# Performance work log

Hardware: AMD Instinct MI355X
Metric: run time of the kernel (lower is better)

Reference implementation:

```python
import jax, jax.numpy as jnp
import numpy as np

WS = 12      # window_size
OV = 6       # overlap
STEP = WS - OV
EPS = 1e-5   # LayerNorm eps (torch default)


def setup_inputs() -> dict:
    key = jax.random.key(0)
    ks = jax.random.split(key, 6)
    B, L, H, Dh = 4, 4092, 8, 64
    d_model = H * Dh
    sc = 1.0 / np.sqrt(Dh)
    return {
        "queries": jax.random.normal(ks[0], (B, L, H, Dh), dtype=jnp.float32),
        "keys": jax.random.normal(ks[1], (B, L, H, Dh), dtype=jnp.float32),
        "values": jax.random.normal(ks[2], (B, L, H, Dh), dtype=jnp.float32),
        "Wq": jax.random.normal(ks[3], (Dh, Dh), dtype=jnp.float32) * sc,
        "Wk": jax.random.normal(ks[4], (Dh, Dh), dtype=jnp.float32) * sc,
        "Wv": jax.random.normal(ks[5], (Dh, Dh), dtype=jnp.float32) * sc,
        "gamma": jnp.ones((d_model,), dtype=jnp.float32),
        "beta": jnp.zeros((d_model,), dtype=jnp.float32),
    }


def reference(queries, keys, values, Wq, Wk, Wv, gamma, beta):
    # input layout: [B, L, H, Dh]
    B, L, H, Dh = queries.shape
    nw = (L - OV) // STEP                       # number of windows
    Lc = WS + STEP * (nw - 1)                   # reconstructed length (== L)
    idx = jnp.arange(nw)[:, None] * STEP + jnp.arange(WS)[None, :]  # [nw, WS]

    def windows(x):
        # [B,L,H,Dh] -> [B,H,nw,WS,Dh]
        return jnp.transpose(x, (0, 2, 1, 3))[:, :, idx, :]

    qw, kw, vw = windows(queries), windows(keys), windows(values)
    # per-head-dim linear projections (nn.Linear: x @ W.T)
    Q = jnp.einsum('bhnwd,ed->bhnwe', qw, Wq)
    K = jnp.einsum('bhnwd,ed->bhnwe', kw, Wk)
    V = jnp.einsum('bhnwd,ed->bhnwe', vw, Wv)

    scores = jnp.einsum('bhnqd,bhnkd->bhnqk', Q, K) / jnp.sqrt(jnp.asarray(Dh, Q.dtype))
    attn = jax.nn.softmax(scores, axis=-1)      # [B,H,nw,WS,WS]
    ow = jnp.einsum('bhnqk,bhnkd->bhnqd', attn, V)

    # [B,H,nw,WS,Dh] -> [B,nw,WS,H*Dh]
    attn_out = jnp.transpose(ow, (0, 2, 3, 1, 4)).reshape(B, nw, WS, H * Dh)

    # overlap-add + averaging
    flat_idx = idx.reshape(-1)                  # [nw*WS]
    acc = jnp.zeros((B, Lc, H * Dh), dtype=attn_out.dtype)
    acc = acc.at[:, flat_idx, :].add(attn_out.reshape(B, nw * WS, H * Dh))
    cnt = jnp.zeros((Lc,), dtype=attn_out.dtype).at[flat_idx].add(1.0)
    out = acc / cnt[None, :, None]

    # residual + LayerNorm
    resid = queries.reshape(B, L, H * Dh)
    x = out + resid
    mu = jnp.mean(x, axis=-1, keepdims=True)
    var = jnp.mean((x - mu) ** 2, axis=-1, keepdims=True)
    z = (x - mu) / jnp.sqrt(var + EPS) * gamma + beta
    return z, attn
```

## Files before the change

kernel.cpp:

```cpp
#include <hip/hip_runtime.h>
#include <math.h>

#define B_    4
#define L_    4092
#define H_    8
#define DM    512
#define WS_   12
#define NW    681
#define NC    682
#define EPS_  1e-5f
#define Z_ELEMS (B_*L_*DM)
#define NQUAD 32736

typedef unsigned short u16;

__device__ __forceinline__ u16 f2bf(float f) {
    union { float f; unsigned u; } x; x.f = f;
    unsigned u = x.u;
    return (u16)((u + 0x7FFFu + ((u >> 16) & 1u)) >> 16);
}
__device__ __forceinline__ float bf2f(u16 h) {
    union { unsigned u; float f; } x; x.u = ((unsigned)h) << 16; return x.f;
}

__global__ __launch_bounds__(256) void proj_kernel(
    const float* __restrict__ q, const float* __restrict__ k, const float* __restrict__ v,
    const float* __restrict__ Wq, const float* __restrict__ Wk, const float* __restrict__ Wv,
    float* __restrict__ Qf, float* __restrict__ Kf, u16* __restrict__ Vh)
{
    const int tensor = blockIdx.y;
    const float* __restrict__ X = (tensor == 0) ? q  : (tensor == 1) ? k  : v;
    const float* __restrict__ W = (tensor == 0) ? Wq : (tensor == 1) ? Wk : Wv;
    float* __restrict__ Yf      = (tensor == 0) ? Qf : Kf;
    const bool isV = (tensor == 2);

    const int t = threadIdx.x, lane = t & 63, wv = t >> 6;

    float4 wr[16];
    #pragma unroll
    for (int j = 0; j < 16; ++j)
        wr[j] = *(const float4*)(W + lane * 64 + j * 4);

    __shared__ alignas(16) float Xw[4][4][64];

    const int li = lane >> 4;
    const int lc = (lane & 15) * 4;

    const int waveId = blockIdx.x * 4 + wv;
    for (int qd = waveId; qd < NQUAD; qd += 2048) {
        const int rbase = qd * 4;
        const int r = rbase + li;
        const int bh = r / L_;
        const int l = r - bh * L_;
        const int b = bh >> 3, h = bh & 7;
        const float4 xf = *(const float4*)(X + (((size_t)b * L_ + l) * H_ + h) * 64 + lc);
        *(float4*)&Xw[wv][li][lc] = xf;

        float acc0 = 0.f, acc1 = 0.f, acc2 = 0.f, acc3 = 0.f;
        #pragma unroll
        for (int d4 = 0; d4 < 16; ++d4) {
            const float4 w4 = wr[d4];
            const float4 x0 = *(const float4*)&Xw[wv][0][d4 * 4];
            const float4 x1 = *(const float4*)&Xw[wv][1][d4 * 4];
            const float4 x2 = *(const float4*)&Xw[wv][2][d4 * 4];
            const float4 x3 = *(const float4*)&Xw[wv][3][d4 * 4];
            acc0 += x0.x*w4.x + x0.y*w4.y + x0.z*w4.z + x0.w*w4.w;
            acc1 += x1.x*w4.x + x1.y*w4.y + x1.z*w4.z + x1.w*w4.w;
            acc2 += x2.x*w4.x + x2.y*w4.y + x2.z*w4.z + x2.w*w4.w;
            acc3 += x3.x*w4.x + x3.y*w4.y + x3.z*w4.z + x3.w*w4.w;
        }

        const size_t orow = (size_t)rbase * 64 + lane;
        if (!isV) {
            Yf[orow]       = acc0;
            Yf[orow + 64]  = acc1;
            Yf[orow + 128] = acc2;
            Yf[orow + 192] = acc3;
        } else {
            Vh[orow]       = f2bf(acc0);
            Vh[orow + 64]  = f2bf(acc1);
            Vh[orow + 128] = f2bf(acc2);
            Vh[orow + 192] = f2bf(acc3);
        }
    }
}

__global__ __launch_bounds__(512, 4) void attn_ln_kernel(
    const float* __restrict__ Qf, const float* __restrict__ Kf, const u16* __restrict__ Vh,
    const float* __restrict__ qres, const float* __restrict__ gamma,
    const float* __restrict__ beta, float* __restrict__ attn, float* __restrict__ z)
{
    __shared__ alignas(16) float Ks[8][18][64];
    __shared__ alignas(16) float Vsf[8][18][64];

    const int c = blockIdx.x, b = blockIdx.y;
    const int t = threadIdx.x, lane = t & 63, h = t >> 6;
    const int qq = lane >> 2, ks = lane & 3;
    const int bh = b * 8 + h;
    const int lbase = c * 6 - 6;

    for (int i = t; i < 2304; i += 512) {
        const int hh  = i / 288;
        const int rem = i - hh * 288;
        const int rr  = rem >> 4;
        const int cc  = (rem & 15) * 4;
        const int l = lbase + rr;
        float4 kf4 = make_float4(0.f, 0.f, 0.f, 0.f);
        float4 vf4 = make_float4(0.f, 0.f, 0.f, 0.f);
        if (l >= 0 && l < L_) {
            const size_t base = ((size_t)(b * 8 + hh) * L_ + l) * 64 + cc;
            kf4 = *(const float4*)(Kf + base);
            const ushort4 u4 = *(const ushort4*)(Vh + base);
            vf4.x = bf2f(u4.x); vf4.y = bf2f(u4.y); vf4.z = bf2f(u4.z); vf4.w = bf2f(u4.w);
        }
        *(float4*)&Ks[hh][rr][cc]  = kf4;
        *(float4*)&Vsf[hh][rr][cc] = vf4;
    }
    __syncthreads();

    const bool hasA = (c < NW), hasB = (c > 0);
    const float scale = (hasA && hasB) ? 0.5f : 1.0f;

    float4 qs0, qs1, qs2, qs3;
    const int qmax = hasA ? 12 : 6;
    if (qq < qmax) {
        const float* qp = Qf + ((size_t)bh * L_ + (c * 6 + qq)) * 64 + ks * 16;
        qs0 = *(const float4*)(qp);     qs1 = *(const float4*)(qp + 4);
        qs2 = *(const float4*)(qp + 8); qs3 = *(const float4*)(qp + 12);
    } else {
        qs0 = qs1 = qs2 = qs3 = make_float4(0.f, 0.f, 0.f, 0.f);
    }

    float s[18];
    #pragma unroll
    for (int kt = 0; kt < 18; ++kt) {
        const float* kp = &Ks[h][kt][ks * 16];
        const float4 k0 = *(const float4*)(kp);
        const float4 k1 = *(const float4*)(kp + 4);
        const float4 k2 = *(const float4*)(kp + 8);
        const float4 k3 = *(const float4*)(kp + 12);
        s[kt] = qs0.x*k0.x + qs0.y*k0.y + qs0.z*k0.z + qs0.w*k0.w
              + qs1.x*k1.x + qs1.y*k1.y + qs1.z*k1.z + qs1.w*k1.w
              + qs2.x*k2.x + qs2.y*k2.y + qs2.z*k2.z + qs2.w*k2.w
              + qs3.x*k3.x + qs3.y*k3.y + qs3.z*k3.z + qs3.w*k3.w;
    }
    #pragma unroll
    for (int kt = 0; kt < 18; ++kt) {
        s[kt] += __shfl_xor(s[kt], 1);
        s[kt] += __shfl_xor(s[kt], 2);
    }

    float eA[12], invA = 0.f;
    if (hasA) {
        float mxA = s[6];
        #pragma unroll
        for (int j = 1; j < 12; ++j) mxA = fmaxf(mxA, s[6 + j]);
        float sumA = 0.f;
        #pragma unroll
        for (int j = 0; j < 12; ++j) { eA[j] = __expf((s[6 + j] - mxA) * 0.125f); sumA += eA[j]; }
        invA = 1.0f / sumA;
        if (ks == 0 && qq < 12) {
            float* ao = attn + ((size_t)bh * NW + c) * 144 + qq * 12;
            float4 a0, a1, a2;
            a0.x = eA[0]*invA; a0.y = eA[1]*invA;  a0.z = eA[2]*invA;  a0.w = eA[3]*invA;
            a1.x = eA[4]*invA; a1.y = eA[5]*invA;  a1.z = eA[6]*invA;  a1.w = eA[7]*invA;
            a2.x = eA[8]*invA; a2.y = eA[9]*invA;  a2.z = eA[10]*invA; a2.w = eA[11]*invA;
            *(float4*)(ao)     = a0;
            *(float4*)(ao + 4) = a1;
            *(float4*)(ao + 8) = a2;
        }
    } else {
        #pragma unroll
        for (int j = 0; j < 12; ++j) eA[j] = 0.f;
    }

    float eB[12], invB = 0.f;
    if (hasB) {
        float mxB = s[0];
        #pragma unroll
        for (int j = 1; j < 12; ++j) mxB = fmaxf(mxB, s[j]);
        float sumB = 0.f;
        #pragma unroll
        for (int j = 0; j < 12; ++j) { eB[j] = __expf((s[j] - mxB) * 0.125f); sumB += eB[j]; }
        invB = 1.0f / sumB;
    } else {
        #pragma unroll
        for (int j = 0; j < 12; ++j) eB[j] = 0.f;
    }

    float4 xo0 = make_float4(0.f,0.f,0.f,0.f), xo1 = xo0, xo2 = xo0, xo3 = xo0;
    if (qq < 6) {
        #pragma unroll
        for (int kt = 0; kt < 18; ++kt) {
            const float wa = (kt >= 6) ? eA[kt - 6] * invA : 0.f;
            const float wb = (kt < 12) ? eB[kt] * invB : 0.f;
            const float wk = scale * (wa + wb);
            const float* vp = &Vsf[h][kt][ks * 16];
            const float4 v0 = *(const float4*)(vp);
            const float4 v1 = *(const float4*)(vp + 4);
            const float4 v2 = *(const float4*)(vp + 8);
            const float4 v3 = *(const float4*)(vp + 12);
            xo0.x += wk*v0.x; xo0.y += wk*v0.y; xo0.z += wk*v0.z; xo0.w += wk*v0.w;
            xo1.x += wk*v1.x; xo1.y += wk*v1.y; xo1.z += wk*v1.z; xo1.w += wk*v1.w;
            xo2.x += wk*v2.x; xo2.y += wk*v2.y; xo2.z += wk*v2.z; xo2.w += wk*v2.w;
            xo3.x += wk*v3.x; xo3.y += wk*v3.y; xo3.z += wk*v3.z; xo3.w += wk*v3.w;
        }
    }
    __syncthreads();

    float* Xs = &Ks[0][0][0];
    if (qq < 6) {
        float* xp = Xs + qq * 516 + h * 64 + ks * 16;
        *(float4*)(xp)      = xo0;
        *(float4*)(xp + 4)  = xo1;
        *(float4*)(xp + 8)  = xo2;
        *(float4*)(xp + 12) = xo3;
    }
    __syncthreads();

    if (h < 6) {
        const int l = c * 6 + h;
        const int cc = lane * 8;
        float4 xa = *(const float4*)(Xs + h * 516 + cc);
        float4 xb = *(const float4*)(Xs + h * 516 + cc + 4);
        const float* qr = qres + ((size_t)b * L_ + l) * DM + cc;
        const float4 ra  = *(const float4*)qr;
        const float4 rb2 = *(const float4*)(qr + 4);
        xa.x += ra.x;  xa.y += ra.y;  xa.z += ra.z;  xa.w += ra.w;
        xb.x += rb2.x; xb.y += rb2.y; xb.z += rb2.z; xb.w += rb2.w;

        float s1 = xa.x + xa.y + xa.z + xa.w + xb.x + xb.y + xb.z + xb.w;
        float s2 = xa.x*xa.x + xa.y*xa.y + xa.z*xa.z + xa.w*xa.w
                 + xb.x*xb.x + xb.y*xb.y + xb.z*xb.z + xb.w*xb.w;
        #pragma unroll
        for (int off = 1; off < 64; off <<= 1) {
            s1 += __shfl_xor(s1, off, 64);
            s2 += __shfl_xor(s2, off, 64);
        }
        const float mu  = s1 * (1.0f / 512.0f);
        const float var = s2 * (1.0f / 512.0f) - mu * mu;
        const float inv = 1.0f / sqrtf(var + EPS_);

        const float4 ga = *(const float4*)(gamma + cc);
        const float4 gb = *(const float4*)(gamma + cc + 4);
        const float4 ba = *(const float4*)(beta + cc);
        const float4 bb = *(const float4*)(beta + cc + 4);
        float4 oa, ob;
        oa.x = (xa.x - mu) * inv * ga.x + ba.x;
        oa.y = (xa.y - mu) * inv * ga.y + ba.y;
        oa.z = (xa.z - mu) * inv * ga.z + ba.z;
        oa.w = (xa.w - mu) * inv * ga.w + ba.w;
        ob.x = (xb.x - mu) * inv * gb.x + bb.x;
        ob.y = (xb.y - mu) * inv * gb.y + bb.y;
        ob.z = (xb.z - mu) * inv * gb.z + bb.z;
        ob.w = (xb.w - mu) * inv * gb.w + bb.w;
        float* zp = z + ((size_t)b * L_ + l) * DM + cc;
        *(float4*)zp = oa;
        *(float4*)(zp + 4) = ob;
    }
}

extern "C" void kernel_launch(void* const* d_in, const int* in_sizes, int n_in,
                              void* d_out, int out_size, void* d_ws, size_t ws_size,
                              hipStream_t stream) {
    const float* q     = (const float*)d_in[0];
    const float* k     = (const float*)d_in[1];
    const float* v     = (const float*)d_in[2];
    const float* Wq    = (const float*)d_in[3];
    const float* Wk    = (const float*)d_in[4];
    const float* Wv    = (const float*)d_in[5];
    const float* gamma = (const float*)d_in[6];
    const float* beta  = (const float*)d_in[7];

    float* z    = (float*)d_out;
    float* attn = (float*)d_out + Z_ELEMS;

    const size_t plane = (size_t)B_ * H_ * L_ * 64;
    float* Qf = (float*)d_ws;
    float* Kf = Qf + plane;
    u16*  Vh  = (u16*)(Kf + plane);

    proj_kernel<<<dim3(512, 3, 1), 256, 0, stream>>>(q, k, v, Wq, Wk, Wv, Qf, Kf, Vh);
    attn_ln_kernel<<<dim3(NC, B_), 512, 0, stream>>>(Qf, Kf, Vh, q, gamma, beta, attn, z);
}
```

Baseline: 247.5 us.

## Drop LDS staging of K/V in attention and restructure projection weight loading

The attention kernel no longer stages K and V tiles in shared memory. Each thread now reads K (fp32) and V (bf16, as 8-wide vectors) straight from global memory, clamping out-of-range rows instead of zero-filling them, which removes the staging loop and two block barriers. The projection kernel transposes W through LDS so each lane holds one output column in 64 registers, reads X rows directly from global as wave-uniform broadcast loads, and launches half as many blocks with a higher occupancy hint. The cost is more redundant global/L2 traffic for K/V rows shared by neighbouring chunks, and higher register pressure in the projection kernel.

```diff
diff --git a/kernel.cpp b/kernel.cpp
--- a/kernel.cpp
+++ b/kernel.cpp
@@ -13,6 +13,7 @@
 #define NQUAD 32736
 
 typedef unsigned short u16;
+typedef __attribute__((ext_vector_type(8))) unsigned short ushort8v;
 
 __device__ __forceinline__ u16 f2bf(float f) {
     union { float f; unsigned u; } x; x.f = f;
@@ -23,11 +24,13 @@
     union { unsigned u; float f; } x; x.u = ((unsigned)h) << 16; return x.f;
 }
 
-__global__ __launch_bounds__(256) void proj_kernel(
+__global__ __launch_bounds__(256, 4) void proj_kernel(
     const float* __restrict__ q, const float* __restrict__ k, const float* __restrict__ v,
     const float* __restrict__ Wq, const float* __restrict__ Wk, const float* __restrict__ Wv,
     float* __restrict__ Qf, float* __restrict__ Kf, u16* __restrict__ Vh)
 {
+    __shared__ float Wt[64][65];
+
     const int tensor = blockIdx.y;
     const float* __restrict__ X = (tensor == 0) ? q  : (tensor == 1) ? k  : v;
     const float* __restrict__ W = (tensor == 0) ? Wq : (tensor == 1) ? Wk : Wv;
@@ -36,38 +39,37 @@
 
     const int t = threadIdx.x, lane = t & 63, wv = t >> 6;
 
-    float4 wr[16];
+    for (int i = t; i < 4096; i += 256) {
+        const int r = i >> 6, cidx = i & 63;
+        Wt[cidx][r] = W[i];
+    }
+    __syncthreads();
+
+    float wr[64];
     #pragma unroll
-    for (int j = 0; j < 16; ++j)
-        wr[j] = *(const float4*)(W + lane * 64 + j * 4);
-
-    __shared__ alignas(16) float Xw[4][4][64];
-
-    const int li = lane >> 4;
-    const int lc = (lane & 15) * 4;
+    for (int d = 0; d < 64; ++d) wr[d] = Wt[d][lane];
 
     const int waveId = blockIdx.x * 4 + wv;
-    for (int qd = waveId; qd < NQUAD; qd += 2048) {
+    for (int qd = waveId; qd < NQUAD; qd += 1024) {
         const int rbase = qd * 4;
-        const int r = rbase + li;
-        const int bh = r / L_;
-        const int l = r - bh * L_;
+        const int bh = rbase / L_;
+        const int l0 = rbase - bh * L_;
         const int b = bh >> 3, h = bh & 7;
-        const float4 xf = *(const float4*)(X + (((size_t)b * L_ + l) * H_ + h) * 64 + lc);
-        *(float4*)&Xw[wv][li][lc] = xf;
+        const float* xr = X + (((size_t)b * L_ + l0) * H_ + h) * 64;
 
         float acc0 = 0.f, acc1 = 0.f, acc2 = 0.f, acc3 = 0.f;
         #pragma unroll
         for (int d4 = 0; d4 < 16; ++d4) {
-            const float4 w4 = wr[d4];
-            const float4 x0 = *(const float4*)&Xw[wv][0][d4 * 4];
-            const float4 x1 = *(const float4*)&Xw[wv][1][d4 * 4];
-            const float4 x2 = *(const float4*)&Xw[wv][2][d4 * 4];
-            const float4 x3 = *(const float4*)&Xw[wv][3][d4 * 4];
-            acc0 += x0.x*w4.x + x0.y*w4.y + x0.z*w4.z + x0.w*w4.w;
-            acc1 += x1.x*w4.x + x1.y*w4.y + x1.z*w4.z + x1.w*w4.w;
-            acc2 += x2.x*w4.x + x2.y*w4.y + x2.z*w4.z + x2.w*w4.w;
-            acc3 += x3.x*w4.x + x3.y*w4.y + x3.z*w4.z + x3.w*w4.w;
+            const float4 x0 = *(const float4*)(xr + d4 * 4);
+            const float4 x1 = *(const float4*)(xr + 512 + d4 * 4);
+            const float4 x2 = *(const float4*)(xr + 1024 + d4 * 4);
+            const float4 x3 = *(const float4*)(xr + 1536 + d4 * 4);
+            const float w0 = wr[4 * d4 + 0], w1 = wr[4 * d4 + 1];
+            const float w2 = wr[4 * d4 + 2], w3 = wr[4 * d4 + 3];
+            acc0 += x0.x*w0 + x0.y*w1 + x0.z*w2 + x0.w*w3;
+            acc1 += x1.x*w0 + x1.y*w1 + x1.z*w2 + x1.w*w3;
+            acc2 += x2.x*w0 + x2.y*w1 + x2.z*w2 + x2.w*w3;
+            acc3 += x3.x*w0 + x3.y*w1 + x3.z*w2 + x3.w*w3;
         }
 
         const size_t orow = (size_t)rbase * 64 + lane;
@@ -90,8 +92,7 @@
     const float* __restrict__ qres, const float* __restrict__ gamma,
     const float* __restrict__ beta, float* __restrict__ attn, float* __restrict__ z)
 {
-    __shared__ alignas(16) float Ks[8][18][64];
-    __shared__ alignas(16) float Vsf[8][18][64];
+    __shared__ alignas(16) float Xs[6 * 516];
 
     const int c = blockIdx.x, b = blockIdx.y;
     const int t = threadIdx.x, lane = t & 63, h = t >> 6;
@@ -99,32 +100,17 @@
     const int bh = b * 8 + h;
     const int lbase = c * 6 - 6;
 
-    for (int i = t; i < 2304; i += 512) {
-        const int hh  = i / 288;
-        const int rem = i - hh * 288;
-        const int rr  = rem >> 4;
-        const int cc  = (rem & 15) * 4;
-        const int l = lbase + rr;
-        float4 kf4 = make_float4(0.f, 0.f, 0.f, 0.f);
-        float4 vf4 = make_float4(0.f, 0.f, 0.f, 0.f);
-        if (l >= 0 && l < L_) {
-            const size_t base = ((size_t)(b * 8 + hh) * L_ + l) * 64 + cc;
-            kf4 = *(const float4*)(Kf + base);
-            const ushort4 u4 = *(const ushort4*)(Vh + base);
-            vf4.x = bf2f(u4.x); vf4.y = bf2f(u4.y); vf4.z = bf2f(u4.z); vf4.w = bf2f(u4.w);
-        }
-        *(float4*)&Ks[hh][rr][cc]  = kf4;
-        *(float4*)&Vsf[hh][rr][cc] = vf4;
-    }
-    __syncthreads();
-
     const bool hasA = (c < NW), hasB = (c > 0);
     const float scale = (hasA && hasB) ? 0.5f : 1.0f;
+
+    const float* Qb = Qf + (size_t)bh * L_ * 64;
+    const float* Kb = Kf + (size_t)bh * L_ * 64;
+    const u16*   Vb = Vh + (size_t)bh * L_ * 64;
 
     float4 qs0, qs1, qs2, qs3;
     const int qmax = hasA ? 12 : 6;
     if (qq < qmax) {
-        const float* qp = Qf + ((size_t)bh * L_ + (c * 6 + qq)) * 64 + ks * 16;
+        const float* qp = Qb + (size_t)(c * 6 + qq) * 64 + ks * 16;
         qs0 = *(const float4*)(qp);     qs1 = *(const float4*)(qp + 4);
         qs2 = *(const float4*)(qp + 8); qs3 = *(const float4*)(qp + 12);
     } else {
@@ -134,7 +120,9 @@
     float s[18];
     #pragma unroll
     for (int kt = 0; kt < 18; ++kt) {
-        const float* kp = &Ks[h][kt][ks * 16];
+        int l = lbase + kt;
+        l = (l < 0) ? 0 : ((l >= L_) ? (L_ - 1) : l);
+        const float* kp = Kb + (size_t)l * 64 + ks * 16;
         const float4 k0 = *(const float4*)(kp);
         const float4 k1 = *(const float4*)(kp + 4);
         const float4 k2 = *(const float4*)(kp + 8);
@@ -195,21 +183,21 @@
             const float wa = (kt >= 6) ? eA[kt - 6] * invA : 0.f;
             const float wb = (kt < 12) ? eB[kt] * invB : 0.f;
             const float wk = scale * (wa + wb);
-            const float* vp = &Vsf[h][kt][ks * 16];
-            const float4 v0 = *(const float4*)(vp);
-            const float4 v1 = *(const float4*)(vp + 4);
-            const float4 v2 = *(const float4*)(vp + 8);
-            const float4 v3 = *(const float4*)(vp + 12);
+            int l = lbase + kt;
+            l = (l < 0) ? 0 : ((l >= L_) ? (L_ - 1) : l);
+            const u16* vp = Vb + (size_t)l * 64 + ks * 16;
+            const ushort8v va = *(const ushort8v*)(vp);
+            const ushort8v vb2 = *(const ushort8v*)(vp + 8);
+            float4 v0, v1, v2, v3;
+            v0.x = bf2f(va[0]);  v0.y = bf2f(va[1]);  v0.z = bf2f(va[2]);  v0.w = bf2f(va[3]);
+            v1.x = bf2f(va[4]);  v1.y = bf2f(va[5]);  v1.z = bf2f(va[6]);  v1.w = bf2f(va[7]);
+            v2.x = bf2f(vb2[0]); v2.y = bf2f(vb2[1]); v2.z = bf2f(vb2[2]); v2.w = bf2f(vb2[3]);
+            v3.x = bf2f(vb2[4]); v3.y = bf2f(vb2[5]); v3.z = bf2f(vb2[6]); v3.w = bf2f(vb2[7]);
             xo0.x += wk*v0.x; xo0.y += wk*v0.y; xo0.z += wk*v0.z; xo0.w += wk*v0.w;
             xo1.x += wk*v1.x; xo1.y += wk*v1.y; xo1.z += wk*v1.z; xo1.w += wk*v1.w;
             xo2.x += wk*v2.x; xo2.y += wk*v2.y; xo2.z += wk*v2.z; xo2.w += wk*v2.w;
             xo3.x += wk*v3.x; xo3.y += wk*v3.y; xo3.z += wk*v3.z; xo3.w += wk*v3.w;
         }
-    }
-    __syncthreads();
-
-    float* Xs = &Ks[0][0][0];
-    if (qq < 6) {
         float* xp = Xs + qq * 516 + h * 64 + ks * 16;
         *(float4*)(xp)      = xo0;
         *(float4*)(xp + 4)  = xo1;
@@ -280,6 +268,6 @@
     float* Kf = Qf + plane;
     u16*  Vh  = (u16*)(Kf + plane);
 
-    proj_kernel<<<dim3(512, 3, 1), 256, 0, stream>>>(q, k, v, Wq, Wk, Wv, Qf, Kf, Vh);
+    proj_kernel<<<dim3(256, 3, 1), 256, 0, stream>>>(q, k, v, Wq, Wk, Wv, Qf, Kf, Vh);
     attn_ln_kernel<<<dim3(NC, B_), 512, 0, stream>>>(Qf, Kf, Vh, q, gamma, beta, attn, z);
 }
```

Result: slower. 675.2 us (+172.8%).
